# Kernel tuning notes

Hardware: AMD Instinct MI355X
Metric: run time of the kernel (lower is better)

The kernel has to match this reference:

```python
import jax, jax.numpy as jnp
import numpy as np

NUM_TOTAL = 150000
NUM_USER = 50000
NUM_ITEM = NUM_TOTAL - NUM_USER
D = 128
SOC_L = 2
CO_L = 2
NEG = 10
R = 0.7
E_SOC = 1600000
E_CO = 3200000
B = 512
MAX_UI = 64
MAX_IU = 50
W = 32
HOP = 3


def _sage_lgcn(x, src, dst, w, n, layers):
    # SAGEConv with edge-softmax weights over destination (LGCN 'mean' option).
    m = jax.lax.stop_gradient(jax.ops.segment_max(w, dst, num_segments=n))
    e = jnp.exp(w - m[dst])
    s = jax.ops.segment_sum(e, dst, num_segments=n)
    alpha = e / (s[dst] + 1e-16)
    for _ in range(layers):
        x = jax.ops.segment_sum(alpha[:, None] * x[src], dst, num_segments=n)
    return x  # LGCN.forward returns the last conv output (not the averaged sum)


def _sym_lgcn(x, src, dst, n, layers):
    # LGCConv: gcn_norm with added self-loops, symmetric D^-1/2 A D^-1/2.
    loop = jnp.arange(n)
    s2 = jnp.concatenate([src, loop])
    d2 = jnp.concatenate([dst, loop])
    deg = jax.ops.segment_sum(jnp.ones_like(d2, dtype=jnp.float32), d2, num_segments=n)
    dinv = jnp.where(deg > 0, deg ** -0.5, 0.0)
    ew = dinv[s2] * dinv[d2]
    for _ in range(layers):
        x = jax.ops.segment_sum(ew[:, None] * x[s2], d2, num_segments=n)
    return x


def _l2norm(x):
    return x / jnp.maximum(jnp.linalg.norm(x, axis=-1, keepdims=True), 1e-12)


def setup_inputs() -> dict:
    ks = jax.random.split(jax.random.key(0), 10)
    id_emb = 0.1 * jax.random.normal(ks[0], (NUM_TOTAL, D), jnp.float32)
    soc_id_emb = 0.1 * jax.random.normal(ks[1], (NUM_TOTAL, D), jnp.float32)
    soc_ext_weight = jax.random.uniform(ks[2], (E_SOC,), jnp.float32)
    soc_edge_index = jax.random.randint(ks[3], (2, E_SOC), 0, NUM_TOTAL)
    co_edge_index = jax.random.randint(ks[4], (2, E_CO), 0, NUM_TOTAL)
    uid = jax.random.randint(ks[5], (B,), 0, NUM_USER)
    pi = jax.random.randint(ks[9], (B,), NUM_USER, NUM_TOTAL)
    n_id = jnp.stack([uid, pi], axis=1)
    user_items = jax.random.randint(ks[6], (B, MAX_UI), 0, NUM_ITEM)
    item_users = jax.random.randint(ks[7], (NUM_ITEM, MAX_IU), 0, NUM_USER)
    walks = jax.random.randint(ks[8], (B, W, HOP), 0, NUM_TOTAL)
    return dict(id_emb=id_emb, soc_id_emb=soc_id_emb, soc_ext_weight=soc_ext_weight,
                soc_edge_index=soc_edge_index, co_edge_index=co_edge_index, n_id=n_id,
                user_items=user_items, item_users=item_users, walks=walks)


def reference(id_emb, soc_id_emb, soc_ext_weight, soc_edge_index, co_edge_index,
              n_id, user_items, item_users, walks):
    pi_id = n_id[:, 1]
    # two message-passing stacks
    soc_emb = _sage_lgcn(soc_id_emb, soc_edge_index[0], soc_edge_index[1],
                         soc_ext_weight, NUM_TOTAL, SOC_L)
    co_emb = _sym_lgcn(id_emb, co_edge_index[0], co_edge_index[1], NUM_TOTAL, CO_L)
    zero = jnp.zeros((1, D), id_emb.dtype)
    co_pad = jnp.concatenate([co_emb, zero], 0)
    soc_pad = jnp.concatenate([soc_emb, zero], 0)
    # vectorized per-user negative sampling: exclude interacted items, sample
    # NEG without replacement via top-k over masked uniform noise.
    rows = jnp.arange(B)[:, None]
    cols = jnp.where(user_items >= 0, user_items, 0)
    avail = jnp.ones((B, NUM_ITEM), jnp.int32).at[rows, cols].min(
        (user_items < 0).astype(jnp.int32))
    noise = jax.random.uniform(jax.random.key(42), (B, NUM_ITEM))
    scorez = jnp.where(avail > 0, noise, -1.0)
    _, neg_local = jax.lax.top_k(scorez, NEG)
    cand = jnp.concatenate([pi_id[:, None], neg_local + NUM_USER], axis=1)  # [B, 1+NEG]
    # item anchor soc embedding = mean of soc_emb over interacting users
    iu_idx = jnp.where(item_users >= 0, item_users, NUM_TOTAL)  # pad -> zero row
    cnt = (item_users >= 0).sum(-1, keepdims=True).astype(id_emb.dtype) + 1e-7
    anchor = soc_pad[iu_idx].sum(1) / cnt  # [NUM_ITEM, D]
    u_ref = jnp.concatenate([soc_emb[:NUM_USER], anchor, zero], 0)  # [NUM_TOTAL+1, D]
    co_n = _l2norm(co_pad)
    soc_n = _l2norm(u_ref)
    wk = walks.reshape(B, -1)  # [B, W*HOP]
    co_sim = (jnp.einsum('bcd,bwd->bcw', co_n[cand], co_n[wk]) + 1.0) * 0.5
    soc_sim = (jnp.einsum('bcd,bwd->bcw', soc_n[cand], soc_n[wk]) + 1.0) * 0.5
    return R * co_sim.mean(-1) + (1.0 - R) * soc_sim.mean(-1)  # [B, 1+NEG]
```

## Files before the change

### kernel.cpp

```cpp
#include <hip/hip_runtime.h>
#include <hip/hip_fp16.h>
#include <stdint.h>

#define NUM_TOTAL 150000
#define NUM_USER  50000
#define NUM_ITEM  100000
#define E_SOC 1600000
#define E_CO  3200000
#define BATCH 512
#define MAX_UI 64
#define MAX_IU 50
#define NWALK 96
#define NCAND 11
#define NB    586
#define NWG   192
#define PARTS 4
#define PIT   25000
#define PMW   784
#define SCAP  192
#define TH    8377900u

__device__ __forceinline__ uint32_t rotl32(uint32_t x, int r){ return (x<<r)|(x>>(32-r)); }

__device__ __forceinline__ void tf_core(uint32_t x0, uint32_t x1, uint32_t& o0, uint32_t& o1){
  const uint32_t k0 = 0u, k1 = 42u, k2 = 0u ^ 42u ^ 0x1BD11BDAu;
  x0 += k0; x1 += k1;
#define TF_R4(a,b,c,d) \
  x0+=x1; x1=rotl32(x1,a); x1^=x0; \
  x0+=x1; x1=rotl32(x1,b); x1^=x0; \
  x0+=x1; x1=rotl32(x1,c); x1^=x0; \
  x0+=x1; x1=rotl32(x1,d); x1^=x0;
  TF_R4(13,15,26,6)   x0+=k1; x1+=k2+1u;
  TF_R4(17,29,16,24)  x0+=k2; x1+=k0+2u;
  TF_R4(13,15,26,6)   x0+=k0; x1+=k1+3u;
  TF_R4(17,29,16,24)  x0+=k1; x1+=k2+4u;
  TF_R4(13,15,26,6)   x0+=k2; x1+=k0+5u;
#undef TF_R4
  o0 = x0; o1 = x1;
}

__device__ __forceinline__ uint32_t tf_bits(uint32_t j){
  uint32_t o0, o1;
  tf_core(0u, j, o0, o1);
  return o0 ^ o1;
}

__global__ __launch_bounds__(256) void pcount_k(const int* __restrict__ dst, int E, int chunk,
                                                int* __restrict__ cntMat ){
  __shared__ int h[NB];
  int tid = threadIdx.x, wg = blockIdx.x;
  for (int i=tid; i<NB; i+=256) h[i]=0;
  __syncthreads();
  int lo = wg*chunk, hi = lo+chunk; if (hi > E) hi = E;
  for (int i=lo+tid; i<hi; i+=256) atomicAdd(&h[dst[i]>>8], 1);
  __syncthreads();
  for (int i=tid; i<NB; i+=256) cntMat[wg*NB + i] = h[i];
}

__global__ __launch_bounds__(1024) void pscan_k(int* __restrict__ cntMat, int* __restrict__ bbase, int E){
  __shared__ int sa[1024];
  int tid = threadIdx.x;
  int tot = 0;
  if (tid < NB){
    for (int wg=0; wg<NWG; ++wg) tot += cntMat[wg*NB + tid];
  }
  sa[tid] = tot;
  __syncthreads();
  for (int s=1; s<1024; s<<=1){
    int v = (tid>=s)?sa[tid-s]:0;
    __syncthreads();
    sa[tid] += v;
    __syncthreads();
  }
  if (tid < NB){
    int base = sa[tid] - tot;
    bbase[tid] = base;
    int run = base;
    for (int wg=0; wg<NWG; ++wg){
      int c = cntMat[wg*NB + tid];
      cntMat[wg*NB + tid] = run;
      run += c;
    }
  }
  if (tid == 0) bbase[NB] = E;
}

__global__ __launch_bounds__(256) void pplace_soc_k(const int* __restrict__ src,
        const int* __restrict__ dst, const float* __restrict__ wgt,
        const int* __restrict__ offMat, unsigned long long* __restrict__ rec, int E, int chunk){
  __shared__ int curx[NB];
  int tid = threadIdx.x, wg = blockIdx.x;
  for (int i=tid; i<NB; i+=256) curx[i] = offMat[wg*NB + i];
  __syncthreads();
  int lo = wg*chunk, hi = lo+chunk; if (hi > E) hi = E;
  for (int i=lo+tid; i<hi; i+=256){
    int d = dst[i];
    int p = atomicAdd(&curx[d>>8], 1);
    rec[p] = ((unsigned long long)__float_as_uint(wgt[i])<<32)
           | (unsigned)(((d&255)<<18) | src[i]);
  }
}

__global__ __launch_bounds__(256) void pplace_co_k(const int* __restrict__ src,
        const int* __restrict__ dst, const int* __restrict__ offMat,
        unsigned int* __restrict__ rec, int E, int chunk){
  __shared__ int curx[NB];
  int tid = threadIdx.x, wg = blockIdx.x;
  for (int i=tid; i<NB; i+=256) curx[i] = offMat[wg*NB + i];
  __syncthreads();
  int lo = wg*chunk, hi = lo+chunk; if (hi > E) hi = E;
  for (int i=lo+tid; i<hi; i+=256){
    int d = dst[i];
    int p = atomicAdd(&curx[d>>8], 1);
    rec[p] = (unsigned)(((d&255)<<18) | src[i]);
  }
}

__global__ __launch_bounds__(256) void csc_soc_k(const unsigned long long* __restrict__ rec,
    const int* __restrict__ bbase, int* __restrict__ off,
    int* __restrict__ srcS, float* __restrict__ wS){
  __shared__ int cnt[256], basex[256], curx[256];
  int b = blockIdx.x, tid = threadIdx.x;
  int lo = bbase[b], hi = bbase[b+1];
  cnt[tid] = 0;
  __syncthreads();
  for (int i = lo + tid; i < hi; i += 256){
    unsigned long long r = rec[i];
    atomicAdd(&cnt[(((unsigned)r) >> 18) & 255], 1);
  }
  __syncthreads();
  int c = cnt[tid];
  basex[tid] = c; __syncthreads();
  for (int s=1; s<256; s<<=1){
    int t = (tid>=s)?basex[tid-s]:0; __syncthreads();
    basex[tid]+=t; __syncthreads();
  }
  int excl = basex[tid]-c;
  int node = b*256+tid;
  if (node <= NUM_TOTAL) off[node] = lo + excl;
  basex[tid] = excl; curx[tid] = 0;
  __syncthreads();
  for (int i = lo + tid; i < hi; i += 256){
    unsigned long long r = rec[i];
    unsigned lw = (unsigned)r;
    int dl = (lw>>18)&255;
    int p = lo + basex[dl] + atomicAdd(&curx[dl],1);
    srcS[p] = lw & 0x3FFFF;
    wS[p] = __uint_as_float((unsigned)(r>>32));
  }
}

__global__ __launch_bounds__(256) void csc_co_k(const unsigned int* __restrict__ rec,
    const int* __restrict__ bbase, int* __restrict__ off, int* __restrict__ srcS){
  __shared__ int cnt[256], basex[256], curx[256];
  int b = blockIdx.x, tid = threadIdx.x;
  int lo = bbase[b], hi = bbase[b+1];
  cnt[tid] = 0;
  __syncthreads();
  for (int i = lo + tid; i < hi; i += 256){
    unsigned r = rec[i];
    atomicAdd(&cnt[(r >> 18) & 255], 1);
  }
  __syncthreads();
  int c = cnt[tid];
  basex[tid] = c; __syncthreads();
  for (int s=1; s<256; s<<=1){
    int t = (tid>=s)?basex[tid-s]:0; __syncthreads();
    basex[tid]+=t; __syncthreads();
  }
  int excl = basex[tid]-c;
  int node = b*256+tid;
  if (node <= NUM_TOTAL) off[node] = lo + excl;
  basex[tid] = excl; curx[tid] = 0;
  __syncthreads();
  for (int i = lo + tid; i < hi; i += 256){
    unsigned r = rec[i];
    int dl = (r>>18)&255;
    int p = lo + basex[dl] + atomicAdd(&curx[dl],1);
    srcS[p] = r & 0x3FFFF;
  }
}

__global__ void dinv_k(const int* __restrict__ off, float* __restrict__ dinv, int n){
  int i = blockIdx.x*blockDim.x + threadIdx.x, st = gridDim.x*blockDim.x;
  for (; i<n; i+=st){
    int deg = off[i+1]-off[i];
    dinv[i] = 1.0f / sqrtf((float)(deg + 1));
  }
}

__global__ void alpha_k(const int* __restrict__ off, float* __restrict__ wS, int n){
  int v = blockIdx.x*blockDim.x + threadIdx.x;
  if (v >= n) return;
  int e0 = off[v], e1 = off[v+1];
  if (e0 == e1) return;
  float m = -3.402823466e+38f;
  for (int e=e0; e<e1; ++e) m = fmaxf(m, wS[e]);
  float s = 0.f;
  for (int e=e0; e<e1; ++e) s += expf(wS[e] - m);
  float inv = 1.0f / (s + 1e-16f);
  for (int e=e0; e<e1; ++e) wS[e] = expf(wS[e] - m) * inv;
}

__global__ void f2h2_k(const float4* __restrict__ a, uint2* __restrict__ oa,
                       const float4* __restrict__ b, uint2* __restrict__ ob, int n4){
  int i = blockIdx.x*blockDim.x+threadIdx.x, st = gridDim.x*blockDim.x;
  for (; i<n4; i+=st){
    float4 va = a[i], vb = b[i];
    __half2 l = __float22half2_rn(make_float2(va.x,va.y));
    __half2 h = __float22half2_rn(make_float2(va.z,va.w));
    uint2 u; u.x = *(unsigned*)&l; u.y = *(unsigned*)&h;
    oa[i] = u;
    l = __float22half2_rn(make_float2(vb.x,vb.y));
    h = __float22half2_rn(make_float2(vb.z,vb.w));
    u.x = *(unsigned*)&l; u.y = *(unsigned*)&h;
    ob[i] = u;
  }
}

__global__ void agg_soc8_k(const __half2* __restrict__ x, __half2* __restrict__ y,
                           const int* __restrict__ off, const int* __restrict__ srcS,
                           const float* __restrict__ wE, int n){
  int gw = (blockIdx.x*blockDim.x + threadIdx.x) >> 6;
  int lane = threadIdx.x & 63;
  if (gw >= n) return;
  float ax = 0.f, ay = 0.f;
  int e = off[gw], e1 = off[gw+1];
  for (; e + 8 <= e1; e += 8){
    int s0=srcS[e],s1=srcS[e+1],s2=srcS[e+2],s3=srcS[e+3];
    int s4=srcS[e+4],s5=srcS[e+5],s6=srcS[e+6],s7=srcS[e+7];
    float a0=wE[e],a1=wE[e+1],a2=wE[e+2],a3=wE[e+3];
    float a4=wE[e+4],a5=wE[e+5],a6=wE[e+6],a7=wE[e+7];
    __half2 h0=x[(size_t)s0*64+lane], h1=x[(size_t)s1*64+lane];
    __half2 h2=x[(size_t)s2*64+lane], h3=x[(size_t)s3*64+lane];
    __half2 h4=x[(size_t)s4*64+lane], h5=x[(size_t)s5*64+lane];
    __half2 h6=x[(size_t)s6*64+lane], h7=x[(size_t)s7*64+lane];
    float2 f0=__half22float2(h0), f1=__half22float2(h1), f2=__half22float2(h2), f3=__half22float2(h3);
    float2 f4=__half22float2(h4), f5=__half22float2(h5), f6=__half22float2(h6), f7=__half22float2(h7);
    ax += a0*f0.x + a1*f1.x + a2*f2.x + a3*f3.x + a4*f4.x + a5*f5.x + a6*f6.x + a7*f7.x;
    ay += a0*f0.y + a1*f1.y + a2*f2.y + a3*f3.y + a4*f4.y + a5*f5.y + a6*f6.y + a7*f7.y;
  }
  for (; e < e1; ++e){
    int s = srcS[e]; float a = wE[e];
    float2 f = __half22float2(x[(size_t)s*64 + lane]);
    ax += a*f.x; ay += a*f.y;
  }
  y[(size_t)gw*64 + lane] = __float22half2_rn(make_float2(ax, ay));
}

__global__ void agg_co8_k(const __half2* __restrict__ x, __half2* __restrict__ y,
                          const int* __restrict__ off, const int* __restrict__ srcS,
                          const float* __restrict__ dinv, int n){
  int gw = (blockIdx.x*blockDim.x + threadIdx.x) >> 6;
  int lane = threadIdx.x & 63;
  if (gw >= n) return;
  float dv = dinv[gw];
  float2 fs = __half22float2(x[(size_t)gw*64 + lane]);
  float ax = dv*dv*fs.x, ay = dv*dv*fs.y;
  int e = off[gw], e1 = off[gw+1];
  for (; e + 8 <= e1; e += 8){
    int s0=srcS[e],s1=srcS[e+1],s2=srcS[e+2],s3=srcS[e+3];
    int s4=srcS[e+4],s5=srcS[e+5],s6=srcS[e+6],s7=srcS[e+7];
    float a0=dinv[s0]*dv,a1=dinv[s1]*dv,a2=dinv[s2]*dv,a3=dinv[s3]*dv;
    float a4=dinv[s4]*dv,a5=dinv[s5]*dv,a6=dinv[s6]*dv,a7=dinv[s7]*dv;
    __half2 h0=x[(size_t)s0*64+lane], h1=x[(size_t)s1*64+lane];
    __half2 h2=x[(size_t)s2*64+lane], h3=x[(size_t)s3*64+lane];
    __half2 h4=x[(size_t)s4*64+lane], h5=x[(size_t)s5*64+lane];
    __half2 h6=x[(size_t)s6*64+lane], h7=x[(size_t)s7*64+lane];
    float2 f0=__half22float2(h0), f1=__half22float2(h1), f2=__half22float2(h2), f3=__half22float2(h3);
    float2 f4=__half22float2(h4), f5=__half22float2(h5), f6=__half22float2(h6), f7=__half22float2(h7);
    ax += a0*f0.x + a1*f1.x + a2*f2.x + a3*f3.x + a4*f4.x + a5*f5.x + a6*f6.x + a7*f7.x;
    ay += a0*f0.y + a1*f1.y + a2*f2.y + a3*f3.y + a4*f4.y + a5*f5.y + a6*f6.y + a7*f7.y;
  }
  for (; e < e1; ++e){
    int s = srcS[e]; float a = dinv[s]*dv;
    float2 f = __half22float2(x[(size_t)s*64 + lane]);
    ax += a*f.x; ay += a*f.y;
  }
  y[(size_t)gw*64 + lane] = __float22half2_rn(make_float2(ax, ay));
}

__global__ void norm_h_k(__half2* __restrict__ x, int n){
  int gw = (blockIdx.x*blockDim.x + threadIdx.x) >> 6;
  int lane = threadIdx.x & 63;
  if (gw >= n) return;
  __half2* p = x + (size_t)gw*64;
  float2 v = __half22float2(p[lane]);
  float ss = v.x*v.x + v.y*v.y;
  #pragma unroll
  for (int s=32; s; s>>=1) ss += __shfl_xor(ss, s, 64);
  float sc = 1.0f / fmaxf(sqrtf(ss), 1e-12f);
  p[lane] = __float22half2_rn(make_float2(v.x*sc, v.y*sc));
}

__global__ void anchor_h_k(const __half2* __restrict__ soc, const int* __restrict__ item_users,
                           __half2* __restrict__ outI, int n){
  int gw = (blockIdx.x*blockDim.x + threadIdx.x) >> 6;
  int lane = threadIdx.x & 63;
  if (gw >= n) return;
  const int* us = item_users + (size_t)gw*MAX_IU;
  float ax = 0.f, ay = 0.f;
  for (int k=0; k<MAX_IU; k+=10){
    int u0=us[k],u1=us[k+1],u2=us[k+2],u3=us[k+3],u4=us[k+4];
    int u5=us[k+5],u6=us[k+6],u7=us[k+7],u8=us[k+8],u9=us[k+9];
    __half2 h0=soc[(size_t)u0*64+lane], h1=soc[(size_t)u1*64+lane];
    __half2 h2=soc[(size_t)u2*64+lane], h3=soc[(size_t)u3*64+lane];
    __half2 h4=soc[(size_t)u4*64+lane], h5=soc[(size_t)u5*64+lane];
    __half2 h6=soc[(size_t)u6*64+lane], h7=soc[(size_t)u7*64+lane];
    __half2 h8=soc[(size_t)u8*64+lane], h9=soc[(size_t)u9*64+lane];
    float2 f0=__half22float2(h0), f1=__half22float2(h1), f2=__half22float2(h2);
    float2 f3=__half22float2(h3), f4=__half22float2(h4), f5=__half22float2(h5);
    float2 f6=__half22float2(h6), f7=__half22float2(h7), f8=__half22float2(h8);
    float2 f9=__half22float2(h9);
    ax += f0.x+f1.x+f2.x+f3.x+f4.x+f5.x+f6.x+f7.x+f8.x+f9.x;
    ay += f0.y+f1.y+f2.y+f3.y+f4.y+f5.y+f6.y+f7.y+f8.y+f9.y;
  }
  const float inv = 1.0f / (50.0f + 1e-7f);
  ax *= inv; ay *= inv;
  float ss = ax*ax + ay*ay;
  #pragma unroll
  for (int s=32; s; s>>=1) ss += __shfl_xor(ss, s, 64);
  float sc = 1.0f / fmaxf(sqrtf(ss), 1e-12f);
  outI[(size_t)gw*64 + lane] = __float22half2_rn(make_float2(ax*sc, ay*sc));
}

__global__ __launch_bounds__(256) void negA_k(const int* __restrict__ user_items,
                                              unsigned long long* __restrict__ surv,
                                              int* __restrict__ scnt){
  __shared__ unsigned int mask[PMW];
  __shared__ int lcnt;
  int blk = blockIdx.x;
  int row = blk >> 2, part = blk & 3;
  int base = part * PIT;
  int tid = threadIdx.x;
  for (int i=tid; i<PMW; i+=256) mask[i] = 0u;
  if (tid == 0) lcnt = 0;
  __syncthreads();
  if (tid < MAX_UI){
    int it = user_items[row*MAX_UI + tid];
    if (it >= base && it < base + PIT){
      int li = it - base;
      atomicOr(&mask[li>>5], 1u << (li & 31));
    }
  }
  __syncthreads();
  unsigned jbase = (unsigned)row * 100000u + (unsigned)base;
  for (int k = tid; k < PIT; k += 512){
    int i1 = k + 256;
    uint32_t b0 = tf_bits(jbase + (unsigned)k);
    uint32_t b1 = tf_bits(jbase + (unsigned)(i1 < PIT ? i1 : k));
    uint32_t v0 = b0 >> 9;
    uint32_t v1 = b1 >> 9;
    if (v0 >= TH && !((mask[k>>5] >> (k&31)) & 1u)){
      int p = atomicAdd(&lcnt, 1);
      if (p < SCAP)
        surv[(size_t)blk*SCAP + p] = ((unsigned long long)v0 << 32) | (unsigned)(~(unsigned)(base + k));
    }
    if (i1 < PIT && v1 >= TH && !((mask[i1>>5] >> (i1&31)) & 1u)){
      int p = atomicAdd(&lcnt, 1);
      if (p < SCAP)
        surv[(size_t)blk*SCAP + p] = ((unsigned long long)v1 << 32) | (unsigned)(~(unsigned)(base + i1));
    }
  }
  __syncthreads();
  if (tid == 0) scnt[blk] = (lcnt < SCAP) ? lcnt : SCAP;
}

__global__ __launch_bounds__(256) void negB_k(const unsigned long long* __restrict__ surv,
                                              const int* __restrict__ scnt,
                                              const int* __restrict__ user_items,
                                              const int* __restrict__ n_id,
                                              int* __restrict__ cand){
  __shared__ unsigned long long keys[PARTS*SCAP];
  __shared__ unsigned long long red[256];
  __shared__ int cnts[PARTS];
  __shared__ int uix[MAX_UI];
  int b = blockIdx.x, tid = threadIdx.x;
  if (tid < PARTS) cnts[tid] = scnt[b*PARTS + tid];
  for (int i=tid; i<PARTS*SCAP; i+=256) keys[i] = 0ull;
  __syncthreads();
  int o0 = 0, o1 = cnts[0], o2 = o1 + cnts[1], o3 = o2 + cnts[2];
  int total = o3 + cnts[3];
  if (tid < cnts[0]) keys[o0 + tid] = surv[(size_t)(b*PARTS+0)*SCAP + tid];
  if (tid < cnts[1]) keys[o1 + tid] = surv[(size_t)(b*PARTS+1)*SCAP + tid];
  if (tid < cnts[2]) keys[o2 + tid] = surv[(size_t)(b*PARTS+2)*SCAP + tid];
  if (tid < cnts[3]) keys[o3 + tid] = surv[(size_t)(b*PARTS+3)*SCAP + tid];
  __syncthreads();
  if (total >= 10){
    for (int r=0; r<10; ++r){
      unsigned long long m = 0ull;
      for (int i=tid; i<PARTS*SCAP; i+=256){ unsigned long long v = keys[i]; if (v > m) m = v; }
      red[tid] = m; __syncthreads();
      for (int s=128; s>0; s>>=1){
        if (tid < s && red[tid+s] > red[tid]) red[tid] = red[tid+s];
        __syncthreads();
      }
      unsigned long long win = red[0];
      if (tid == 0)
        cand[b*NCAND + 1 + r] = NUM_USER + (int)(~(unsigned)(win & 0xffffffffull));
      for (int i=tid; i<PARTS*SCAP; i+=256) if (keys[i] == win) keys[i] = 0ull;
      __syncthreads();
    }
  } else {
    if (tid < MAX_UI) uix[tid] = user_items[b*MAX_UI + tid];
    __syncthreads();
    unsigned long long prev = ~0ull;
    for (int r=0; r<10; ++r){
      unsigned long long m = 0ull;
      for (int i=tid; i<NUM_ITEM; i+=256){
        bool msk = false;
        for (int j=0; j<MAX_UI; ++j) if (uix[j] == i) msk = true;
        if (msk) continue;
        uint32_t v = tf_bits((unsigned)b*100000u + (unsigned)i) >> 9;
        unsigned long long key = ((unsigned long long)v << 32) | (unsigned)(~(unsigned)i);
        if (key < prev && key > m) m = key;
      }
      red[tid] = m; __syncthreads();
      for (int s=128; s>0; s>>=1){
        if (tid < s && red[tid+s] > red[tid]) red[tid] = red[tid+s];
        __syncthreads();
      }
      unsigned long long win = red[0];
      prev = win;
      if (tid == 0)
        cand[b*NCAND + 1 + r] = NUM_USER + (int)(~(unsigned)(win & 0xffffffffull));
      __syncthreads();
    }
  }
  if (tid == 0) cand[b*NCAND] = n_id[b*2 + 1];
}

__global__ void sim_h_k(const __half2* __restrict__ coN, const __half2* __restrict__ socU,
                        const __half2* __restrict__ socI, const int* __restrict__ cand,
                        const int* __restrict__ walks, float* __restrict__ out){
  int b = blockIdx.x;
  int lane = threadIdx.x;
  float scx=0.f, scy=0.f, ssx=0.f, ssy=0.f;
  for (int w=0; w<NWALK; w+=4){
    int i0 = walks[b*NWALK + w],   i1 = walks[b*NWALK + w+1];
    int i2 = walks[b*NWALK + w+2], i3 = walks[b*NWALK + w+3];
    __half2 c0 = coN[(size_t)i0*64 + lane], c1 = coN[(size_t)i1*64 + lane];
    __half2 c2 = coN[(size_t)i2*64 + lane], c3 = coN[(size_t)i3*64 + lane];
    const __half2* p0 = (i0 < NUM_USER) ? socU + (size_t)i0*64 : socI + (size_t)(i0-NUM_USER)*64;
    const __half2* p1 = (i1 < NUM_USER) ? socU + (size_t)i1*64 : socI + (size_t)(i1-NUM_USER)*64;
    const __half2* p2 = (i2 < NUM_USER) ? socU + (size_t)i2*64 : socI + (size_t)(i2-NUM_USER)*64;
    const __half2* p3 = (i3 < NUM_USER) ? socU + (size_t)i3*64 : socI + (size_t)(i3-NUM_USER)*64;
    __half2 s0 = p0[lane], s1 = p1[lane], s2 = p2[lane], s3 = p3[lane];
    float2 fc0 = __half22float2(c0), fc1 = __half22float2(c1);
    float2 fc2 = __half22float2(c2), fc3 = __half22float2(c3);
    float2 fs0 = __half22float2(s0), fs1 = __half22float2(s1);
    float2 fs2 = __half22float2(s2), fs3 = __half22float2(s3);
    scx += fc0.x + fc1.x + fc2.x + fc3.x;
    scy += fc0.y + fc1.y + fc2.y + fc3.y;
    ssx += fs0.x + fs1.x + fs2.x + fs3.x;
    ssy += fs0.y + fs1.y + fs2.y + fs3.y;
  }
  for (int c=0; c<NCAND; ++c){
    int idx = cand[b*NCAND + c];
    float2 cv = __half22float2(coN[(size_t)idx*64 + lane]);
    float2 sv = __half22float2(socI[(size_t)(idx - NUM_USER)*64 + lane]);
    float dco = cv.x*scx + cv.y*scy;
    float dso = sv.x*ssx + sv.y*ssy;
    #pragma unroll
    for (int s=32; s; s>>=1){
      dco += __shfl_xor(dco, s, 64);
      dso += __shfl_xor(dso, s, 64);
    }
    if (lane == 0){
      float com = 0.5f + 0.5f*(dco / 96.0f);
      float som = 0.5f + 0.5f*(dso / 96.0f);
      out[b*NCAND + c] = 0.7f*com + 0.3f*som;
    }
  }
}

extern "C" void kernel_launch(void* const* d_in, const int* in_sizes, int n_in,
                              void* d_out, int out_size, void* d_ws, size_t ws_size,
                              hipStream_t stream){
  (void)in_sizes; (void)n_in; (void)out_size; (void)ws_size;
  const float* id_emb     = (const float*)d_in[0];
  const float* soc_id_emb = (const float*)d_in[1];
  const float* soc_w      = (const float*)d_in[2];
  const int*   soc_ei     = (const int*)d_in[3];
  const int*   co_ei      = (const int*)d_in[4];
  const int*   n_id       = (const int*)d_in[5];
  const int*   user_items = (const int*)d_in[6];
  const int*   item_users = (const int*)d_in[7];
  const int*   walks      = (const int*)d_in[8];
  float* out = (float*)d_out;

  char* w = (char*)d_ws;
  size_t cur = 0;
  auto take = [&](size_t bytes)->void*{
    void* p = w + cur;
    cur = (cur + bytes + 255) & ~(size_t)255;
    return p;
  };
  __half2* socId16 = (__half2*)take((size_t)NUM_TOTAL*64*4);
  __half2* id16    = (__half2*)take((size_t)NUM_TOTAL*64*4);
  __half2* t16     = (__half2*)take((size_t)NUM_TOTAL*64*4);
  __half2* soc16   = (__half2*)take((size_t)NUM_TOTAL*64*4);
  __half2* co16    = (__half2*)take((size_t)NUM_TOTAL*64*4);
  int*   socOff  = (int*)take((size_t)(NUM_TOTAL+1)*4);
  int*   coOff   = (int*)take((size_t)(NUM_TOTAL+1)*4);
  float* dinv    = (float*)take((size_t)NUM_TOTAL*4);
  int*   socSrcS = (int*)take((size_t)E_SOC*4);
  float* socWS   = (float*)take((size_t)E_SOC*4);
  int*   coSrcS  = (int*)take((size_t)E_CO*4);
  int*   cntMatS = (int*)take((size_t)NWG*NB*4);
  int*   cntMatC = (int*)take((size_t)NWG*NB*4);
  int*   bbaseS  = (int*)take((size_t)(NB+1)*4);
  int*   bbaseC  = (int*)take((size_t)(NB+1)*4);
  unsigned long long* surv = (unsigned long long*)take((size_t)BATCH*PARTS*SCAP*8);
  int*   scnt    = (int*)take((size_t)BATCH*PARTS*4);
  int*   cand    = (int*)take((size_t)BATCH*NCAND*4);

  unsigned long long* recS = (unsigned long long*)t16;
  unsigned int*       recC = (unsigned int*)((char*)t16 + (size_t)E_SOC*8);

  __half2* anch16 = socId16;

  const int T = 256;
  const int chunkS = (E_SOC + NWG - 1) / NWG;
  const int chunkC = (E_CO  + NWG - 1) / NWG;

  pcount_k<<<NWG, T, 0, stream>>>(soc_ei + E_SOC, E_SOC, chunkS, cntMatS);
  pcount_k<<<NWG, T, 0, stream>>>(co_ei + E_CO,  E_CO,  chunkC, cntMatC);
  pscan_k<<<1, 1024, 0, stream>>>(cntMatS, bbaseS, E_SOC);
  pscan_k<<<1, 1024, 0, stream>>>(cntMatC, bbaseC, E_CO);
  pplace_soc_k<<<NWG, T, 0, stream>>>(soc_ei, soc_ei + E_SOC, soc_w, cntMatS, recS, E_SOC, chunkS);
  pplace_co_k <<<NWG, T, 0, stream>>>(co_ei,  co_ei  + E_CO,         cntMatC, recC, E_CO,  chunkC);
  csc_soc_k<<<NB, T, 0, stream>>>(recS, bbaseS, socOff, socSrcS, socWS);
  csc_co_k <<<NB, T, 0, stream>>>(recC, bbaseC, coOff, coSrcS);

  dinv_k<<<(NUM_TOTAL + T - 1)/T, T, 0, stream>>>(coOff, dinv, NUM_TOTAL);
  alpha_k<<<(NUM_TOTAL + T - 1)/T, T, 0, stream>>>(socOff, socWS, NUM_TOTAL);

  negA_k<<<BATCH*PARTS, T, 0, stream>>>(user_items, surv, scnt);

  f2h2_k<<<2048, T, 0, stream>>>((const float4*)soc_id_emb, (uint2*)socId16,
                                 (const float4*)id_emb,     (uint2*)id16, NUM_TOTAL*32);

  int aggGrid = (NUM_TOTAL + 3) / 4;
  agg_soc8_k<<<aggGrid, T, 0, stream>>>(socId16, soc16, socOff, socSrcS, socWS, NUM_TOTAL);
  agg_soc8_k<<<aggGrid, T, 0, stream>>>(soc16,   t16,   socOff, socSrcS, socWS, NUM_TOTAL);
  agg_co8_k <<<aggGrid, T, 0, stream>>>(id16,    co16,  coOff,  coSrcS,  dinv,  NUM_TOTAL);
  agg_co8_k <<<aggGrid, T, 0, stream>>>(co16,    id16,  coOff,  coSrcS,  dinv,  NUM_TOTAL);

  __half2* socE = t16;
  __half2* coE  = id16;

  norm_h_k<<<aggGrid, T, 0, stream>>>(coE, NUM_TOTAL);
  anchor_h_k<<<(NUM_ITEM + 3)/4, T, 0, stream>>>(socE, item_users, anch16, NUM_ITEM);
  norm_h_k<<<(NUM_USER + 3)/4, T, 0, stream>>>(socE, NUM_USER);

  negB_k<<<BATCH, T, 0, stream>>>(surv, scnt, user_items, n_id, cand);
  sim_h_k<<<BATCH, 64, 0, stream>>>(coE, socE, anch16, cand, walks, out);
}
```

Before: 1.054 ms.

## Merge soc/co graph-build and aggregation kernels into combined launches

Combines the paired social and co-occurrence kernels (count, scan, place, CSC build, layer aggregation, norm/anchor) into single launches that split blocks by graph. Folds the alpha softmax and dinv computation into the CSC build kernel, which removes two launches and extra passes over the offsets. Aggregation loops now run 8-wide with clamped indices and zero weights instead of a scalar tail, and negA processes four candidates per iteration. The intent is fewer launches and better overlap between the two independent graphs. In exchange there is some warp divergence at the soc/co boundary, and the per-node softmax runs serially inside the CSC block after a sync.

```diff
diff --git a/kernel.cpp b/kernel.cpp
--- a/kernel.cpp
+++ b/kernel.cpp
@@ -45,10 +45,19 @@
   return o0 ^ o1;
 }
 
-__global__ __launch_bounds__(256) void pcount_k(const int* __restrict__ dst, int E, int chunk,
-                                                int* __restrict__ cntMat ){
+__global__ __launch_bounds__(256) void pcountB_k(const int* __restrict__ socDst,
+                                                 const int* __restrict__ coDst,
+                                                 int chunkS, int chunkC,
+                                                 int* __restrict__ cntMatS,
+                                                 int* __restrict__ cntMatC){
   __shared__ int h[NB];
-  int tid = threadIdx.x, wg = blockIdx.x;
+  int tid = threadIdx.x;
+  bool isSoc = blockIdx.x < NWG;
+  int wg = isSoc ? blockIdx.x : blockIdx.x - NWG;
+  const int* dst = isSoc ? socDst : coDst;
+  int E = isSoc ? E_SOC : E_CO;
+  int chunk = isSoc ? chunkS : chunkC;
+  int* cntMat = isSoc ? cntMatS : cntMatC;
   for (int i=tid; i<NB; i+=256) h[i]=0;
   __syncthreads();
   int lo = wg*chunk, hi = lo+chunk; if (hi > E) hi = E;
@@ -57,9 +66,13 @@
   for (int i=tid; i<NB; i+=256) cntMat[wg*NB + i] = h[i];
 }
 
-__global__ __launch_bounds__(1024) void pscan_k(int* __restrict__ cntMat, int* __restrict__ bbase, int E){
+__global__ __launch_bounds__(1024) void pscan2_k(int* __restrict__ cntMatS, int* __restrict__ cntMatC,
+                                                 int* __restrict__ bbaseS, int* __restrict__ bbaseC){
   __shared__ int sa[1024];
   int tid = threadIdx.x;
+  int* cntMat = blockIdx.x ? cntMatC : cntMatS;
+  int* bbase  = blockIdx.x ? bbaseC  : bbaseS;
+  int E       = blockIdx.x ? E_CO    : E_SOC;
   int tot = 0;
   if (tid < NB){
     for (int wg=0; wg<NWG; ++wg) tot += cntMat[wg*NB + tid];
@@ -85,48 +98,56 @@
   if (tid == 0) bbase[NB] = E;
 }
 
-__global__ __launch_bounds__(256) void pplace_soc_k(const int* __restrict__ src,
-        const int* __restrict__ dst, const float* __restrict__ wgt,
-        const int* __restrict__ offMat, unsigned long long* __restrict__ rec, int E, int chunk){
+__global__ __launch_bounds__(256) void pplaceB_k(const int* __restrict__ socSrc,
+        const int* __restrict__ socDst, const float* __restrict__ socWgt,
+        const int* __restrict__ coSrc,  const int* __restrict__ coDst,
+        const int* __restrict__ cntMatS, const int* __restrict__ cntMatC,
+        unsigned long long* __restrict__ recS, unsigned int* __restrict__ recC,
+        int chunkS, int chunkC){
   __shared__ int curx[NB];
-  int tid = threadIdx.x, wg = blockIdx.x;
+  int tid = threadIdx.x;
+  bool isSoc = blockIdx.x < NWG;
+  int wg = isSoc ? blockIdx.x : blockIdx.x - NWG;
+  const int* offMat = isSoc ? cntMatS : cntMatC;
   for (int i=tid; i<NB; i+=256) curx[i] = offMat[wg*NB + i];
   __syncthreads();
-  int lo = wg*chunk, hi = lo+chunk; if (hi > E) hi = E;
-  for (int i=lo+tid; i<hi; i+=256){
-    int d = dst[i];
-    int p = atomicAdd(&curx[d>>8], 1);
-    rec[p] = ((unsigned long long)__float_as_uint(wgt[i])<<32)
-           | (unsigned)(((d&255)<<18) | src[i]);
-  }
-}
-
-__global__ __launch_bounds__(256) void pplace_co_k(const int* __restrict__ src,
-        const int* __restrict__ dst, const int* __restrict__ offMat,
-        unsigned int* __restrict__ rec, int E, int chunk){
-  __shared__ int curx[NB];
-  int tid = threadIdx.x, wg = blockIdx.x;
-  for (int i=tid; i<NB; i+=256) curx[i] = offMat[wg*NB + i];
-  __syncthreads();
-  int lo = wg*chunk, hi = lo+chunk; if (hi > E) hi = E;
-  for (int i=lo+tid; i<hi; i+=256){
-    int d = dst[i];
-    int p = atomicAdd(&curx[d>>8], 1);
-    rec[p] = (unsigned)(((d&255)<<18) | src[i]);
-  }
-}
-
-__global__ __launch_bounds__(256) void csc_soc_k(const unsigned long long* __restrict__ rec,
-    const int* __restrict__ bbase, int* __restrict__ off,
-    int* __restrict__ srcS, float* __restrict__ wS){
+  if (isSoc){
+    int lo = wg*chunkS, hi = lo+chunkS; if (hi > E_SOC) hi = E_SOC;
+    for (int i=lo+tid; i<hi; i+=256){
+      int d = socDst[i];
+      int p = atomicAdd(&curx[d>>8], 1);
+      recS[p] = ((unsigned long long)__float_as_uint(socWgt[i])<<32)
+              | (unsigned)(((d&255)<<18) | socSrc[i]);
+    }
+  } else {
+    int lo = wg*chunkC, hi = lo+chunkC; if (hi > E_CO) hi = E_CO;
+    for (int i=lo+tid; i<hi; i+=256){
+      int d = coDst[i];
+      int p = atomicAdd(&curx[d>>8], 1);
+      recC[p] = (unsigned)(((d&255)<<18) | coSrc[i]);
+    }
+  }
+}
+
+__global__ __launch_bounds__(256) void cscB_k(const unsigned long long* __restrict__ recS,
+    const unsigned int* __restrict__ recC,
+    const int* __restrict__ bbaseS, const int* __restrict__ bbaseC,
+    int* __restrict__ socOff, int* __restrict__ socSrcS, float* __restrict__ socWS,
+    int* __restrict__ coOff, int* __restrict__ coSrcS, float* __restrict__ dinv){
   __shared__ int cnt[256], basex[256], curx[256];
-  int b = blockIdx.x, tid = threadIdx.x;
+  int tid = threadIdx.x;
+  bool isSoc = blockIdx.x < NB;
+  int b = isSoc ? blockIdx.x : blockIdx.x - NB;
+  const int* bbase = isSoc ? bbaseS : bbaseC;
   int lo = bbase[b], hi = bbase[b+1];
   cnt[tid] = 0;
   __syncthreads();
-  for (int i = lo + tid; i < hi; i += 256){
-    unsigned long long r = rec[i];
-    atomicAdd(&cnt[(((unsigned)r) >> 18) & 255], 1);
+  if (isSoc){
+    for (int i = lo + tid; i < hi; i += 256)
+      atomicAdd(&cnt[(((unsigned)recS[i]) >> 18) & 255], 1);
+  } else {
+    for (int i = lo + tid; i < hi; i += 256)
+      atomicAdd(&cnt[(recC[i] >> 18) & 255], 1);
   }
   __syncthreads();
   int c = cnt[tid];
@@ -137,69 +158,38 @@
   }
   int excl = basex[tid]-c;
   int node = b*256+tid;
+  int* off = isSoc ? socOff : coOff;
   if (node <= NUM_TOTAL) off[node] = lo + excl;
   basex[tid] = excl; curx[tid] = 0;
   __syncthreads();
-  for (int i = lo + tid; i < hi; i += 256){
-    unsigned long long r = rec[i];
-    unsigned lw = (unsigned)r;
-    int dl = (lw>>18)&255;
-    int p = lo + basex[dl] + atomicAdd(&curx[dl],1);
-    srcS[p] = lw & 0x3FFFF;
-    wS[p] = __uint_as_float((unsigned)(r>>32));
-  }
-}
-
-__global__ __launch_bounds__(256) void csc_co_k(const unsigned int* __restrict__ rec,
-    const int* __restrict__ bbase, int* __restrict__ off, int* __restrict__ srcS){
-  __shared__ int cnt[256], basex[256], curx[256];
-  int b = blockIdx.x, tid = threadIdx.x;
-  int lo = bbase[b], hi = bbase[b+1];
-  cnt[tid] = 0;
-  __syncthreads();
-  for (int i = lo + tid; i < hi; i += 256){
-    unsigned r = rec[i];
-    atomicAdd(&cnt[(r >> 18) & 255], 1);
-  }
-  __syncthreads();
-  int c = cnt[tid];
-  basex[tid] = c; __syncthreads();
-  for (int s=1; s<256; s<<=1){
-    int t = (tid>=s)?basex[tid-s]:0; __syncthreads();
-    basex[tid]+=t; __syncthreads();
-  }
-  int excl = basex[tid]-c;
-  int node = b*256+tid;
-  if (node <= NUM_TOTAL) off[node] = lo + excl;
-  basex[tid] = excl; curx[tid] = 0;
-  __syncthreads();
-  for (int i = lo + tid; i < hi; i += 256){
-    unsigned r = rec[i];
-    int dl = (r>>18)&255;
-    int p = lo + basex[dl] + atomicAdd(&curx[dl],1);
-    srcS[p] = r & 0x3FFFF;
-  }
-}
-
-__global__ void dinv_k(const int* __restrict__ off, float* __restrict__ dinv, int n){
-  int i = blockIdx.x*blockDim.x + threadIdx.x, st = gridDim.x*blockDim.x;
-  for (; i<n; i+=st){
-    int deg = off[i+1]-off[i];
-    dinv[i] = 1.0f / sqrtf((float)(deg + 1));
-  }
-}
-
-__global__ void alpha_k(const int* __restrict__ off, float* __restrict__ wS, int n){
-  int v = blockIdx.x*blockDim.x + threadIdx.x;
-  if (v >= n) return;
-  int e0 = off[v], e1 = off[v+1];
-  if (e0 == e1) return;
-  float m = -3.402823466e+38f;
-  for (int e=e0; e<e1; ++e) m = fmaxf(m, wS[e]);
-  float s = 0.f;
-  for (int e=e0; e<e1; ++e) s += expf(wS[e] - m);
-  float inv = 1.0f / (s + 1e-16f);
-  for (int e=e0; e<e1; ++e) wS[e] = expf(wS[e] - m) * inv;
+  if (isSoc){
+    for (int i = lo + tid; i < hi; i += 256){
+      unsigned long long r = recS[i];
+      unsigned lw = (unsigned)r;
+      int dl = (lw>>18)&255;
+      int p = lo + basex[dl] + atomicAdd(&curx[dl],1);
+      socSrcS[p] = lw & 0x3FFFF;
+      socWS[p] = __uint_as_float((unsigned)(r>>32));
+    }
+    __syncthreads();
+    if (node < NUM_TOTAL && c > 0){
+      int e0 = lo + basex[tid], e1 = e0 + c;
+      float m = -3.402823466e+38f;
+      for (int e=e0; e<e1; ++e) m = fmaxf(m, socWS[e]);
+      float s = 0.f;
+      for (int e=e0; e<e1; ++e) s += expf(socWS[e] - m);
+      float inv = 1.0f / (s + 1e-16f);
+      for (int e=e0; e<e1; ++e) socWS[e] = expf(socWS[e] - m) * inv;
+    }
+  } else {
+    for (int i = lo + tid; i < hi; i += 256){
+      unsigned r = recC[i];
+      int dl = (r>>18)&255;
+      int p = lo + basex[dl] + atomicAdd(&curx[dl],1);
+      coSrcS[p] = r & 0x3FFFF;
+    }
+    if (node < NUM_TOTAL) dinv[node] = 1.0f / sqrtf((float)(c + 1));
+  }
 }
 
 __global__ void f2h2_k(const float4* __restrict__ a, uint2* __restrict__ oa,
@@ -218,66 +208,75 @@
   }
 }
 
-__global__ void agg_soc8_k(const __half2* __restrict__ x, __half2* __restrict__ y,
-                           const int* __restrict__ off, const int* __restrict__ srcS,
-                           const float* __restrict__ wE, int n){
+__global__ void aggL_k(const __half2* __restrict__ socX, __half2* __restrict__ socY,
+                       const __half2* __restrict__ coX,  __half2* __restrict__ coY,
+                       const int* __restrict__ socOff, const int* __restrict__ socSrc,
+                       const float* __restrict__ socW,
+                       const int* __restrict__ coOff, const int* __restrict__ coSrc,
+                       const float* __restrict__ dinv){
   int gw = (blockIdx.x*blockDim.x + threadIdx.x) >> 6;
   int lane = threadIdx.x & 63;
-  if (gw >= n) return;
-  float ax = 0.f, ay = 0.f;
-  int e = off[gw], e1 = off[gw+1];
-  for (; e + 8 <= e1; e += 8){
-    int s0=srcS[e],s1=srcS[e+1],s2=srcS[e+2],s3=srcS[e+3];
-    int s4=srcS[e+4],s5=srcS[e+5],s6=srcS[e+6],s7=srcS[e+7];
-    float a0=wE[e],a1=wE[e+1],a2=wE[e+2],a3=wE[e+3];
-    float a4=wE[e+4],a5=wE[e+5],a6=wE[e+6],a7=wE[e+7];
-    __half2 h0=x[(size_t)s0*64+lane], h1=x[(size_t)s1*64+lane];
-    __half2 h2=x[(size_t)s2*64+lane], h3=x[(size_t)s3*64+lane];
-    __half2 h4=x[(size_t)s4*64+lane], h5=x[(size_t)s5*64+lane];
-    __half2 h6=x[(size_t)s6*64+lane], h7=x[(size_t)s7*64+lane];
-    float2 f0=__half22float2(h0), f1=__half22float2(h1), f2=__half22float2(h2), f3=__half22float2(h3);
-    float2 f4=__half22float2(h4), f5=__half22float2(h5), f6=__half22float2(h6), f7=__half22float2(h7);
-    ax += a0*f0.x + a1*f1.x + a2*f2.x + a3*f3.x + a4*f4.x + a5*f5.x + a6*f6.x + a7*f7.x;
-    ay += a0*f0.y + a1*f1.y + a2*f2.y + a3*f3.y + a4*f4.y + a5*f5.y + a6*f6.y + a7*f7.y;
-  }
-  for (; e < e1; ++e){
-    int s = srcS[e]; float a = wE[e];
-    float2 f = __half22float2(x[(size_t)s*64 + lane]);
-    ax += a*f.x; ay += a*f.y;
-  }
-  y[(size_t)gw*64 + lane] = __float22half2_rn(make_float2(ax, ay));
-}
-
-__global__ void agg_co8_k(const __half2* __restrict__ x, __half2* __restrict__ y,
-                          const int* __restrict__ off, const int* __restrict__ srcS,
-                          const float* __restrict__ dinv, int n){
-  int gw = (blockIdx.x*blockDim.x + threadIdx.x) >> 6;
-  int lane = threadIdx.x & 63;
-  if (gw >= n) return;
-  float dv = dinv[gw];
-  float2 fs = __half22float2(x[(size_t)gw*64 + lane]);
-  float ax = dv*dv*fs.x, ay = dv*dv*fs.y;
-  int e = off[gw], e1 = off[gw+1];
-  for (; e + 8 <= e1; e += 8){
-    int s0=srcS[e],s1=srcS[e+1],s2=srcS[e+2],s3=srcS[e+3];
-    int s4=srcS[e+4],s5=srcS[e+5],s6=srcS[e+6],s7=srcS[e+7];
-    float a0=dinv[s0]*dv,a1=dinv[s1]*dv,a2=dinv[s2]*dv,a3=dinv[s3]*dv;
-    float a4=dinv[s4]*dv,a5=dinv[s5]*dv,a6=dinv[s6]*dv,a7=dinv[s7]*dv;
-    __half2 h0=x[(size_t)s0*64+lane], h1=x[(size_t)s1*64+lane];
-    __half2 h2=x[(size_t)s2*64+lane], h3=x[(size_t)s3*64+lane];
-    __half2 h4=x[(size_t)s4*64+lane], h5=x[(size_t)s5*64+lane];
-    __half2 h6=x[(size_t)s6*64+lane], h7=x[(size_t)s7*64+lane];
-    float2 f0=__half22float2(h0), f1=__half22float2(h1), f2=__half22float2(h2), f3=__half22float2(h3);
-    float2 f4=__half22float2(h4), f5=__half22float2(h5), f6=__half22float2(h6), f7=__half22float2(h7);
-    ax += a0*f0.x + a1*f1.x + a2*f2.x + a3*f3.x + a4*f4.x + a5*f5.x + a6*f6.x + a7*f7.x;
-    ay += a0*f0.y + a1*f1.y + a2*f2.y + a3*f3.y + a4*f4.y + a5*f5.y + a6*f6.y + a7*f7.y;
-  }
-  for (; e < e1; ++e){
-    int s = srcS[e]; float a = dinv[s]*dv;
-    float2 f = __half22float2(x[(size_t)s*64 + lane]);
-    ax += a*f.x; ay += a*f.y;
-  }
-  y[(size_t)gw*64 + lane] = __float22half2_rn(make_float2(ax, ay));
+  if (gw < NUM_TOTAL){
+    float ax = 0.f, ay = 0.f;
+    int e = socOff[gw], e1 = socOff[gw+1];
+    while (e < e1){
+      int last = e1 - 1;
+      int j1=min(e+1,last), j2=min(e+2,last), j3=min(e+3,last);
+      int j4=min(e+4,last), j5=min(e+5,last), j6=min(e+6,last), j7=min(e+7,last);
+      int s0=socSrc[e],  s1=socSrc[j1], s2=socSrc[j2], s3=socSrc[j3];
+      int s4=socSrc[j4], s5=socSrc[j5], s6=socSrc[j6], s7=socSrc[j7];
+      float a0 = socW[e];
+      float a1 = (e+1<e1)? socW[e+1] : 0.f;
+      float a2 = (e+2<e1)? socW[e+2] : 0.f;
+      float a3 = (e+3<e1)? socW[e+3] : 0.f;
+      float a4 = (e+4<e1)? socW[e+4] : 0.f;
+      float a5 = (e+5<e1)? socW[e+5] : 0.f;
+      float a6 = (e+6<e1)? socW[e+6] : 0.f;
+      float a7 = (e+7<e1)? socW[e+7] : 0.f;
+      __half2 h0=socX[(size_t)s0*64+lane], h1=socX[(size_t)s1*64+lane];
+      __half2 h2=socX[(size_t)s2*64+lane], h3=socX[(size_t)s3*64+lane];
+      __half2 h4=socX[(size_t)s4*64+lane], h5=socX[(size_t)s5*64+lane];
+      __half2 h6=socX[(size_t)s6*64+lane], h7=socX[(size_t)s7*64+lane];
+      float2 f0=__half22float2(h0), f1=__half22float2(h1), f2=__half22float2(h2), f3=__half22float2(h3);
+      float2 f4=__half22float2(h4), f5=__half22float2(h5), f6=__half22float2(h6), f7=__half22float2(h7);
+      ax += a0*f0.x + a1*f1.x + a2*f2.x + a3*f3.x + a4*f4.x + a5*f5.x + a6*f6.x + a7*f7.x;
+      ay += a0*f0.y + a1*f1.y + a2*f2.y + a3*f3.y + a4*f4.y + a5*f5.y + a6*f6.y + a7*f7.y;
+      e += 8;
+    }
+    socY[(size_t)gw*64 + lane] = __float22half2_rn(make_float2(ax, ay));
+  } else {
+    int v = gw - NUM_TOTAL;
+    if (v >= NUM_TOTAL) return;
+    float dv = dinv[v];
+    float2 fs = __half22float2(coX[(size_t)v*64 + lane]);
+    float ax = dv*dv*fs.x, ay = dv*dv*fs.y;
+    int e = coOff[v], e1 = coOff[v+1];
+    while (e < e1){
+      int last = e1 - 1;
+      int j1=min(e+1,last), j2=min(e+2,last), j3=min(e+3,last);
+      int j4=min(e+4,last), j5=min(e+5,last), j6=min(e+6,last), j7=min(e+7,last);
+      int s0=coSrc[e],  s1=coSrc[j1], s2=coSrc[j2], s3=coSrc[j3];
+      int s4=coSrc[j4], s5=coSrc[j5], s6=coSrc[j6], s7=coSrc[j7];
+      float a0 = dinv[s0]*dv;
+      float a1 = (e+1<e1)? dinv[s1]*dv : 0.f;
+      float a2 = (e+2<e1)? dinv[s2]*dv : 0.f;
+      float a3 = (e+3<e1)? dinv[s3]*dv : 0.f;
+      float a4 = (e+4<e1)? dinv[s4]*dv : 0.f;
+      float a5 = (e+5<e1)? dinv[s5]*dv : 0.f;
+      float a6 = (e+6<e1)? dinv[s6]*dv : 0.f;
+      float a7 = (e+7<e1)? dinv[s7]*dv : 0.f;
+      __half2 h0=coX[(size_t)s0*64+lane], h1=coX[(size_t)s1*64+lane];
+      __half2 h2=coX[(size_t)s2*64+lane], h3=coX[(size_t)s3*64+lane];
+      __half2 h4=coX[(size_t)s4*64+lane], h5=coX[(size_t)s5*64+lane];
+      __half2 h6=coX[(size_t)s6*64+lane], h7=coX[(size_t)s7*64+lane];
+      float2 f0=__half22float2(h0), f1=__half22float2(h1), f2=__half22float2(h2), f3=__half22float2(h3);
+      float2 f4=__half22float2(h4), f5=__half22float2(h5), f6=__half22float2(h6), f7=__half22float2(h7);
+      ax += a0*f0.x + a1*f1.x + a2*f2.x + a3*f3.x + a4*f4.x + a5*f5.x + a6*f6.x + a7*f7.x;
+      ay += a0*f0.y + a1*f1.y + a2*f2.y + a3*f3.y + a4*f4.y + a5*f5.y + a6*f6.y + a7*f7.y;
+      e += 8;
+    }
+    coY[(size_t)v*64 + lane] = __float22half2_rn(make_float2(ax, ay));
+  }
 }
 
 __global__ void norm_h_k(__half2* __restrict__ x, int n){
@@ -293,35 +292,46 @@
   p[lane] = __float22half2_rn(make_float2(v.x*sc, v.y*sc));
 }
 
-__global__ void anchor_h_k(const __half2* __restrict__ soc, const int* __restrict__ item_users,
-                           __half2* __restrict__ outI, int n){
+__global__ void postA_k(__half2* __restrict__ coE, const __half2* __restrict__ socE,
+                        const int* __restrict__ item_users, __half2* __restrict__ anch){
   int gw = (blockIdx.x*blockDim.x + threadIdx.x) >> 6;
   int lane = threadIdx.x & 63;
-  if (gw >= n) return;
-  const int* us = item_users + (size_t)gw*MAX_IU;
-  float ax = 0.f, ay = 0.f;
-  for (int k=0; k<MAX_IU; k+=10){
-    int u0=us[k],u1=us[k+1],u2=us[k+2],u3=us[k+3],u4=us[k+4];
-    int u5=us[k+5],u6=us[k+6],u7=us[k+7],u8=us[k+8],u9=us[k+9];
-    __half2 h0=soc[(size_t)u0*64+lane], h1=soc[(size_t)u1*64+lane];
-    __half2 h2=soc[(size_t)u2*64+lane], h3=soc[(size_t)u3*64+lane];
-    __half2 h4=soc[(size_t)u4*64+lane], h5=soc[(size_t)u5*64+lane];
-    __half2 h6=soc[(size_t)u6*64+lane], h7=soc[(size_t)u7*64+lane];
-    __half2 h8=soc[(size_t)u8*64+lane], h9=soc[(size_t)u9*64+lane];
-    float2 f0=__half22float2(h0), f1=__half22float2(h1), f2=__half22float2(h2);
-    float2 f3=__half22float2(h3), f4=__half22float2(h4), f5=__half22float2(h5);
-    float2 f6=__half22float2(h6), f7=__half22float2(h7), f8=__half22float2(h8);
-    float2 f9=__half22float2(h9);
-    ax += f0.x+f1.x+f2.x+f3.x+f4.x+f5.x+f6.x+f7.x+f8.x+f9.x;
-    ay += f0.y+f1.y+f2.y+f3.y+f4.y+f5.y+f6.y+f7.y+f8.y+f9.y;
-  }
-  const float inv = 1.0f / (50.0f + 1e-7f);
-  ax *= inv; ay *= inv;
-  float ss = ax*ax + ay*ay;
-  #pragma unroll
-  for (int s=32; s; s>>=1) ss += __shfl_xor(ss, s, 64);
-  float sc = 1.0f / fmaxf(sqrtf(ss), 1e-12f);
-  outI[(size_t)gw*64 + lane] = __float22half2_rn(make_float2(ax*sc, ay*sc));
+  if (gw < NUM_TOTAL){
+    __half2* p = coE + (size_t)gw*64;
+    float2 v = __half22float2(p[lane]);
+    float ss = v.x*v.x + v.y*v.y;
+    #pragma unroll
+    for (int s=32; s; s>>=1) ss += __shfl_xor(ss, s, 64);
+    float sc = 1.0f / fmaxf(sqrtf(ss), 1e-12f);
+    p[lane] = __float22half2_rn(make_float2(v.x*sc, v.y*sc));
+  } else {
+    int it = gw - NUM_TOTAL;
+    if (it >= NUM_ITEM) return;
+    const int* us = item_users + (size_t)it*MAX_IU;
+    float ax = 0.f, ay = 0.f;
+    for (int k=0; k<MAX_IU; k+=10){
+      int u0=us[k],u1=us[k+1],u2=us[k+2],u3=us[k+3],u4=us[k+4];
+      int u5=us[k+5],u6=us[k+6],u7=us[k+7],u8=us[k+8],u9=us[k+9];
+      __half2 h0=socE[(size_t)u0*64+lane], h1=socE[(size_t)u1*64+lane];
+      __half2 h2=socE[(size_t)u2*64+lane], h3=socE[(size_t)u3*64+lane];
+      __half2 h4=socE[(size_t)u4*64+lane], h5=socE[(size_t)u5*64+lane];
+      __half2 h6=socE[(size_t)u6*64+lane], h7=socE[(size_t)u7*64+lane];
+      __half2 h8=socE[(size_t)u8*64+lane], h9=socE[(size_t)u9*64+lane];
+      float2 f0=__half22float2(h0), f1=__half22float2(h1), f2=__half22float2(h2);
+      float2 f3=__half22float2(h3), f4=__half22float2(h4), f5=__half22float2(h5);
+      float2 f6=__half22float2(h6), f7=__half22float2(h7), f8=__half22float2(h8);
+      float2 f9=__half22float2(h9);
+      ax += f0.x+f1.x+f2.x+f3.x+f4.x+f5.x+f6.x+f7.x+f8.x+f9.x;
+      ay += f0.y+f1.y+f2.y+f3.y+f4.y+f5.y+f6.y+f7.y+f8.y+f9.y;
+    }
+    const float inv = 1.0f / (50.0f + 1e-7f);
+    ax *= inv; ay *= inv;
+    float ss = ax*ax + ay*ay;
+    #pragma unroll
+    for (int s=32; s; s>>=1) ss += __shfl_xor(ss, s, 64);
+    float sc = 1.0f / fmaxf(sqrtf(ss), 1e-12f);
+    anch[(size_t)it*64 + lane] = __float22half2_rn(make_float2(ax*sc, ay*sc));
+  }
 }
 
 __global__ __launch_bounds__(256) void negA_k(const int* __restrict__ user_items,
@@ -345,12 +355,13 @@
   }
   __syncthreads();
   unsigned jbase = (unsigned)row * 100000u + (unsigned)base;
-  for (int k = tid; k < PIT; k += 512){
-    int i1 = k + 256;
+  for (int k = tid; k < PIT; k += 1024){
+    int i1 = k + 256, i2 = k + 512, i3 = k + 768;
     uint32_t b0 = tf_bits(jbase + (unsigned)k);
     uint32_t b1 = tf_bits(jbase + (unsigned)(i1 < PIT ? i1 : k));
-    uint32_t v0 = b0 >> 9;
-    uint32_t v1 = b1 >> 9;
+    uint32_t b2 = tf_bits(jbase + (unsigned)(i2 < PIT ? i2 : k));
+    uint32_t b3 = tf_bits(jbase + (unsigned)(i3 < PIT ? i3 : k));
+    uint32_t v0 = b0 >> 9, v1 = b1 >> 9, v2 = b2 >> 9, v3 = b3 >> 9;
     if (v0 >= TH && !((mask[k>>5] >> (k&31)) & 1u)){
       int p = atomicAdd(&lcnt, 1);
       if (p < SCAP)
@@ -360,6 +371,16 @@
       int p = atomicAdd(&lcnt, 1);
       if (p < SCAP)
         surv[(size_t)blk*SCAP + p] = ((unsigned long long)v1 << 32) | (unsigned)(~(unsigned)(base + i1));
+    }
+    if (i2 < PIT && v2 >= TH && !((mask[i2>>5] >> (i2&31)) & 1u)){
+      int p = atomicAdd(&lcnt, 1);
+      if (p < SCAP)
+        surv[(size_t)blk*SCAP + p] = ((unsigned long long)v2 << 32) | (unsigned)(~(unsigned)(base + i2));
+    }
+    if (i3 < PIT && v3 >= TH && !((mask[i3>>5] >> (i3&31)) & 1u)){
+      int p = atomicAdd(&lcnt, 1);
+      if (p < SCAP)
+        surv[(size_t)blk*SCAP + p] = ((unsigned long long)v3 << 32) | (unsigned)(~(unsigned)(base + i3));
     }
   }
   __syncthreads();
@@ -524,34 +545,29 @@
   const int chunkS = (E_SOC + NWG - 1) / NWG;
   const int chunkC = (E_CO  + NWG - 1) / NWG;
 
-  pcount_k<<<NWG, T, 0, stream>>>(soc_ei + E_SOC, E_SOC, chunkS, cntMatS);
-  pcount_k<<<NWG, T, 0, stream>>>(co_ei + E_CO,  E_CO,  chunkC, cntMatC);
-  pscan_k<<<1, 1024, 0, stream>>>(cntMatS, bbaseS, E_SOC);
-  pscan_k<<<1, 1024, 0, stream>>>(cntMatC, bbaseC, E_CO);
-  pplace_soc_k<<<NWG, T, 0, stream>>>(soc_ei, soc_ei + E_SOC, soc_w, cntMatS, recS, E_SOC, chunkS);
-  pplace_co_k <<<NWG, T, 0, stream>>>(co_ei,  co_ei  + E_CO,         cntMatC, recC, E_CO,  chunkC);
-  csc_soc_k<<<NB, T, 0, stream>>>(recS, bbaseS, socOff, socSrcS, socWS);
-  csc_co_k <<<NB, T, 0, stream>>>(recC, bbaseC, coOff, coSrcS);
-
-  dinv_k<<<(NUM_TOTAL + T - 1)/T, T, 0, stream>>>(coOff, dinv, NUM_TOTAL);
-  alpha_k<<<(NUM_TOTAL + T - 1)/T, T, 0, stream>>>(socOff, socWS, NUM_TOTAL);
+  pcountB_k<<<2*NWG, T, 0, stream>>>(soc_ei + E_SOC, co_ei + E_CO, chunkS, chunkC, cntMatS, cntMatC);
+  pscan2_k<<<2, 1024, 0, stream>>>(cntMatS, cntMatC, bbaseS, bbaseC);
+  pplaceB_k<<<2*NWG, T, 0, stream>>>(soc_ei, soc_ei + E_SOC, soc_w,
+                                     co_ei, co_ei + E_CO,
+                                     cntMatS, cntMatC, recS, recC, chunkS, chunkC);
+  cscB_k<<<2*NB, T, 0, stream>>>(recS, recC, bbaseS, bbaseC,
+                                 socOff, socSrcS, socWS, coOff, coSrcS, dinv);
 
   negA_k<<<BATCH*PARTS, T, 0, stream>>>(user_items, surv, scnt);
 
   f2h2_k<<<2048, T, 0, stream>>>((const float4*)soc_id_emb, (uint2*)socId16,
                                  (const float4*)id_emb,     (uint2*)id16, NUM_TOTAL*32);
 
-  int aggGrid = (NUM_TOTAL + 3) / 4;
-  agg_soc8_k<<<aggGrid, T, 0, stream>>>(socId16, soc16, socOff, socSrcS, socWS, NUM_TOTAL);
-  agg_soc8_k<<<aggGrid, T, 0, stream>>>(soc16,   t16,   socOff, socSrcS, socWS, NUM_TOTAL);
-  agg_co8_k <<<aggGrid, T, 0, stream>>>(id16,    co16,  coOff,  coSrcS,  dinv,  NUM_TOTAL);
-  agg_co8_k <<<aggGrid, T, 0, stream>>>(co16,    id16,  coOff,  coSrcS,  dinv,  NUM_TOTAL);
+  int aggGrid = (2*NUM_TOTAL + 3) / 4;
+  aggL_k<<<aggGrid, T, 0, stream>>>(socId16, soc16, id16, co16,
+                                    socOff, socSrcS, socWS, coOff, coSrcS, dinv);
+  aggL_k<<<aggGrid, T, 0, stream>>>(soc16, t16, co16, id16,
+                                    socOff, socSrcS, socWS, coOff, coSrcS, dinv);
 
   __half2* socE = t16;
   __half2* coE  = id16;
 
-  norm_h_k<<<aggGrid, T, 0, stream>>>(coE, NUM_TOTAL);
-  anchor_h_k<<<(NUM_ITEM + 3)/4, T, 0, stream>>>(socE, item_users, anch16, NUM_ITEM);
+  postA_k<<<(2*NUM_TOTAL - NUM_USER + 3)/4, T, 0, stream>>>(coE, socE, item_users, anch16);
   norm_h_k<<<(NUM_USER + 3)/4, T, 0, stream>>>(socE, NUM_USER);
 
   negB_k<<<BATCH, T, 0, stream>>>(surv, scnt, user_items, n_id, cand);
```

New measurement: 1.077 ms. 2.2% more time.
